# Kernel tuning notes

Measured on AMD Instinct MI355X. Metric: run time of the kernel, lower is better.

The kernel has to match this reference:

```python
import jax, jax.numpy as jnp
import numpy as np

B, L, V, E, RV, RD, H, C = 128, 256, 6000, 128, 300, 100, 256, 33
PAD, START, END = 0, 31, 32
DIN = E + 3 * RD  # 428, LSTM input size


def setup_inputs() -> dict:
    key = jax.random.key(0)
    ks = jax.random.split(key, 16)
    def n(k, shape, scale=0.05):
        return jax.random.normal(k, shape, jnp.float32) * scale
    batch_data = jax.random.randint(ks[0], (B, L), 0, V)
    batch_onerad = jax.random.randint(ks[1], (3, B, L), 0, RV)
    lengths = jax.random.randint(ks[2], (B,), L // 2, L + 1)
    tags = jax.random.randint(ks[3], (B, L), 1, C - 2)  # real tags, exclude PAD/START/END
    batch_tag = jnp.where(jnp.arange(L)[None, :] < lengths[:, None], tags, PAD)
    return dict(
        batch_data=batch_data, batch_onerad=batch_onerad, batch_tag=batch_tag,
        embed=n(ks[4], (V, E), 1.0), rad_embed=n(ks[5], (RV, RD), 1.0),
        Wih_f=n(ks[6], (4 * H, DIN)), Whh_f=n(ks[7], (4 * H, H)),
        bih_f=n(ks[8], (4 * H,)), bhh_f=n(ks[9], (4 * H,)),
        Wih_b=n(ks[10], (4 * H, DIN)), Whh_b=n(ks[11], (4 * H, H)),
        bih_b=n(ks[12], (4 * H,)), bhh_b=n(ks[13], (4 * H,)),
        Wcls=n(ks[14], (C, 2 * H)), bcls=n(ks[15], (C,)),
        transition=jnp.full((C, C), 1.0 / C, jnp.float32),
    )


def _lstm_dir(x, Wih, Whh, bih, bhh, reverse):
    # x: [B,L,D] -> h: [B,L,H]; PyTorch gate order i,f,g,o
    xg = jnp.einsum('bld,gd->blg', x, Wih) + bih + bhh  # [B,L,4H]
    xg = jnp.swapaxes(xg, 0, 1)  # [L,B,4H]
    h0 = jnp.zeros((x.shape[0], Whh.shape[1]), x.dtype)
    def step(carry, g):
        h, c = carry
        g = g + h @ Whh.T
        i, f, gg, o = jnp.split(g, 4, axis=-1)
        c = jax.nn.sigmoid(f) * c + jax.nn.sigmoid(i) * jnp.tanh(gg)
        h = jax.nn.sigmoid(o) * jnp.tanh(c)
        return (h, c), h
    _, hs = jax.lax.scan(step, (h0, h0), xg, reverse=reverse)
    return jnp.swapaxes(hs, 0, 1)


def _forward_loss(batch_data, batch_onerad, batch_tag, embed, rad_embed,
                  Wih_f, Whh_f, bih_f, bhh_f, Wih_b, Whh_b, bih_b, bhh_b,
                  Wcls, bcls, transition):
    emb = jnp.concatenate([embed[batch_data], rad_embed[batch_onerad[0]],
                           rad_embed[batch_onerad[1]], rad_embed[batch_onerad[2]]], axis=-1)
    hf = _lstm_dir(emb, Wih_f, Whh_f, bih_f, bhh_f, False)
    hb = _lstm_dir(emb, Wih_b, Whh_b, bih_b, bhh_b, True)
    out = jnp.concatenate([hf, hb], axis=-1)  # [B,L,2H]
    emission = out @ Wcls.T + bcls  # [B,L,C]
    crf_scores = emission[:, :, None, :] + transition  # [B,L,C_prev,C_cur]
    mask = batch_tag != PAD  # [B,L], padding only at the tail
    lengths = mask.sum(axis=1)  # [B]
    # golden path score: index prev*C + cur in flattened [C*C] per step
    prev = jnp.concatenate([jnp.full((B, 1), START, batch_tag.dtype), batch_tag[:, :-1]], axis=1)
    idx = prev * C + batch_tag  # [B,L]
    flat = crf_scores.reshape(B, L, C * C)
    golden = jnp.sum(jnp.take_along_axis(flat, idx[:, :, None], axis=2)[:, :, 0] * mask)
    # CRF forward algorithm (logsumexp scan over time)
    scores0 = jnp.where((lengths > 0)[:, None], crf_scores[:, 0, START, :], 0.0)  # [B,C]
    cs = jnp.swapaxes(crf_scores, 0, 1)[1:]  # [L-1,B,C,C]
    active = jnp.arange(1, L)[:, None] < lengths[None, :]  # [L-1,B]
    def fstep(scores, xs):
        cs_t, act = xs
        new = jax.nn.logsumexp(cs_t + scores[:, :, None], axis=1)  # reduce over prev tag
        return jnp.where(act[:, None], new, scores), None
    scores, _ = jax.lax.scan(fstep, scores0, (cs, active))
    all_path = scores[:, END].sum()
    return (all_path - golden) / B


def reference(batch_data, batch_onerad, batch_tag, embed, rad_embed,
              Wih_f, Whh_f, bih_f, bhh_f, Wih_b, Whh_b, bih_b, bhh_b,
              Wcls, bcls, transition):
    return _forward_loss(batch_data, batch_onerad, batch_tag, embed, rad_embed,
                         Wih_f, Whh_f, bih_f, bhh_f, Wih_b, Whh_b, bih_b, bhh_b,
                         Wcls, bcls, transition)
```

## Files before the change

### kernel.cpp

```cpp
#include <hip/hip_runtime.h>
#include <hip/hip_bf16.h>
#include <stdint.h>


typedef unsigned short u16;
typedef __attribute__((ext_vector_type(8))) __bf16 bf16x8;
typedef __attribute__((ext_vector_type(4))) float f32x4;
typedef __attribute__((ext_vector_type(8))) int i32x8;
typedef __attribute__((ext_vector_type(4))) int i32x4;

struct __align__(8) u16x4 { u16 x, y, z, w; };

typedef const void __attribute__((address_space(1))) gas_t;
typedef void __attribute__((address_space(3))) las_t;

static __device__ __forceinline__ void gload16(const void* g, void* l) {
  __builtin_amdgcn_global_load_lds((gas_t*)g, (las_t*)l, 16, 0, 0);
}

static __device__ __forceinline__ u16 f2b(float x) {
  uint32_t u = __builtin_bit_cast(uint32_t, x);
  uint32_t r = u + 0x7fffu + ((u >> 16) & 1u);
  return (u16)(r >> 16);
}
static __device__ __forceinline__ float b2lo(uint32_t u) {
  return __builtin_bit_cast(float, u << 16);
}
static __device__ __forceinline__ float b2hi(uint32_t u) {
  return __builtin_bit_cast(float, u & 0xffff0000u);
}
static __device__ __forceinline__ uint32_t pkbf16(float lo, float hi) {
  uint32_t w;
  asm("v_cvt_pk_bf16_f32 %0, %1, %2" : "=v"(w) : "v"(lo), "v"(hi));
  return w;
}
static __device__ __forceinline__ uint32_t pkf8x4(float x, float y, float z, float w) {
  unsigned int r01 = __builtin_amdgcn_cvt_pk_fp8_f32(x, y, 0u, false) & 0xffffu;
  unsigned int r23 = __builtin_amdgcn_cvt_pk_fp8_f32(z, w, 0u, false) & 0xffffu;
  return r01 | (r23 << 16);
}
static __device__ __forceinline__ float sigf(float x) {
  return __builtin_amdgcn_rcpf(1.f + __expf(-x));
}
static __device__ __forceinline__ float tanh_(float x) {
  return 1.f - 2.f * __builtin_amdgcn_rcpf(1.f + __expf(2.f * x));
}
static __device__ __forceinline__ f32x4 MFMA(bf16x8 a, bf16x8 b, f32x4 c) {
  return __builtin_amdgcn_mfma_f32_16x16x32_bf16(a, b, c, 0, 0, 0);
}

__global__ __launch_bounds__(256) void pack_all(
    const float* __restrict__ Wih_f, const float* __restrict__ Wih_b,
    const float* __restrict__ Whh_f, const float* __restrict__ Whh_b,
    const float* __restrict__ bih_f, const float* __restrict__ bhh_f,
    const float* __restrict__ bih_b, const float* __restrict__ bhh_b,
    const float* __restrict__ Wcls,
    const int* __restrict__ data, const int* __restrict__ onerad,
    const float* __restrict__ embed, const float* __restrict__ rad,
    unsigned char* __restrict__ W8, unsigned int* __restrict__ WhhF8,
    float* __restrict__ biasP, u16* __restrict__ WclsP,
    unsigned char* __restrict__ A8) {
  if (blockIdx.x < 1640) {
    int idx = blockIdx.x * 256 + threadIdx.x;
    if (idx < 262144) {
      int r = idx >> 7, c7 = idx & 127, k0 = c7 * 4;
      int d = r >> 10, rr = r & 1023;
      const float* W = d ? Wih_b : Wih_f;
      float4 f;
      if (k0 < 428) f = *(const float4*)(W + (size_t)rr * 428 + k0);
      else          f = make_float4(0.f, 0.f, 0.f, 0.f);
      *(unsigned int*)(W8 + (size_t)r * 512 + (k0 ^ ((r & 7) << 4))) =
          pkf8x4(f.x, f.y, f.z, f.w);
    } else if (idx < 264192) {
      int j = idx - 262144;
      int r = j & 1023;
      biasP[j] = (j >> 10) ? (bih_b[r] + bhh_b[r]) : (bih_f[r] + bhh_f[r]);
    } else if (idx < 288768) {
      int j = idx - 264192;
      int r = j >> 9, k = j & 511;
      WclsP[j] = (r < 33) ? f2b(Wcls[r * 512 + k]) : (u16)0;
    } else if (idx < 419840) {
      int q = idx - 288768;
      int f = q >> 9;
      int kt = f & 1, u = (f >> 1) & 7, v = (f >> 4) & 7, dd = f >> 7;
      int w9 = q & 511;
      int lane = w9 >> 3;
      int eb = (w9 & 7) * 4;
      int gate = u >> 1, jf = u & 1;
      int gcol = gate * 256 + v * 32 + jf * 16 + (lane & 15);
      int k = kt * 128 + (lane >> 4) * 32 + eb;
      const float* W = dd ? Whh_b : Whh_f;
      float4 fv4 = *(const float4*)(W + (size_t)gcol * 256 + k);
      WhhF8[q] = pkf8x4(fv4.x, fv4.y, fv4.z, fv4.w);
    }
  } else {
    int idx = (blockIdx.x - 1640) * 256 + threadIdx.x;
    int m = idx >> 7, c = idx & 127, k0 = c * 4;
    float4 vv;
    if (k0 < 128)      vv = *(const float4*)(embed + (size_t)data[m] * 128 + k0);
    else if (k0 < 228) vv = *(const float4*)(rad + (size_t)onerad[m] * 100 + (k0 - 128));
    else if (k0 < 328) vv = *(const float4*)(rad + (size_t)onerad[32768 + m] * 100 + (k0 - 228));
    else if (k0 < 428) vv = *(const float4*)(rad + (size_t)onerad[65536 + m] * 100 + (k0 - 328));
    else               vv = make_float4(0.f, 0.f, 0.f, 0.f);
    *(unsigned int*)(A8 + (size_t)m * 512 + (k0 ^ ((m & 7) << 4))) =
        pkf8x4(vv.x, vv.y, vv.z, vv.w);
  }
}

#define GXM(i, j) \
  acc[i][j] = __builtin_amdgcn_mfma_scale_f32_16x16x128_f8f6f4( \
      af[i], bfj, acc[i][j], 0, 0, 0, 0x7F7F7F7Fu, 0, 0x7F7F7F7Fu);
__global__ __launch_bounds__(256, 2) void gemm_xg(const unsigned char* __restrict__ A8,
    const unsigned char* __restrict__ W8, const float* __restrict__ bias,
    u16* __restrict__ X2) {
  __shared__ unsigned char As[16384];
  __shared__ unsigned char Bs[16384];
  int bid = blockIdx.x;
  int mt = bid >> 4, nt = bid & 15;
  int m0 = mt * 128, n0 = nt * 128;
  int tid = threadIdx.x;
  int w = tid >> 6, lane = tid & 63, l16 = lane & 15;
  int wr = w >> 1, wc = w & 1;
  int kc0 = (lane >> 4) * 32;
  f32x4 zero4 = {0.f, 0.f, 0.f, 0.f};
  f32x4 acc[4][4];
#pragma unroll
  for (int i = 0; i < 4; ++i)
#pragma unroll
    for (int j = 0; j < 4; ++j) acc[i][j] = zero4;
  for (int kk = 0; kk < 4; ++kk) {
    int kb = kk * 128;
#pragma unroll
    for (int ps = 0; ps < 4; ++ps) {
      int o = ps * 4096 + tid * 16;
      int rs = o >> 7, cb = o & 127;
      gload16(A8 + (size_t)(m0 + rs) * 512 + kb + cb, (char*)As + o);
      gload16(W8 + (size_t)(n0 + rs) * 512 + kb + cb, (char*)Bs + o);
    }
    __syncthreads();
    i32x8 af[4];
#pragma unroll
    for (int i = 0; i < 4; ++i) {
      int arow = wr * 64 + i * 16 + l16;
      int sw = (arow & 7) << 4;
      const unsigned char* ab = As + arow * 128;
      i32x4 x0 = *(const i32x4*)(ab + (kc0 ^ sw));
      i32x4 x1 = *(const i32x4*)(ab + ((kc0 + 16) ^ sw));
      af[i] = (i32x8){x0[0], x0[1], x0[2], x0[3], x1[0], x1[1], x1[2], x1[3]};
    }
#pragma unroll
    for (int j = 0; j < 4; ++j) {
      int brow = wc * 64 + j * 16 + l16;
      int sw = (brow & 7) << 4;
      const unsigned char* bb = Bs + brow * 128;
      i32x4 y0 = *(const i32x4*)(bb + (kc0 ^ sw));
      i32x4 y1 = *(const i32x4*)(bb + ((kc0 + 16) ^ sw));
      i32x8 bfj = (i32x8){y0[0], y0[1], y0[2], y0[3], y1[0], y1[1], y1[2], y1[3]};
      GXM(0, j) GXM(1, j) GXM(2, j) GXM(3, j)
    }
    __syncthreads();
  }
  float bv[4];
#pragma unroll
  for (int j = 0; j < 4; ++j) bv[j] = bias[n0 + wc * 64 + j * 16 + l16];
  int dd = n0 >> 10;
  int g = lane >> 4;
#pragma unroll
  for (int i = 0; i < 4; ++i)
#pragma unroll
    for (int jp = 0; jp < 2; ++jp) {
      int j0 = jp * 2;
      int c = (n0 + wc * 64 + j0 * 16 + l16) & 1023;
      int gate = c >> 8, vv = (c >> 5) & 7, lc = c & 15;
      size_t base = (size_t)dd * 33554432 + (size_t)gate * 256 + vv * 32 + lc * 2;
#pragma unroll
      for (int r = 0; r < 4; ++r) {
        int row = m0 + wr * 64 + i * 16 + g * 4 + r;
        *(unsigned int*)(X2 + base + (size_t)row * 1024) =
            pkbf16(acc[i][j0][r] + bv[j0], acc[i][j0 + 1][r] + bv[j0 + 1]);
      }
    }
}

#define MXM(u, Af, Bf) \
  acc[u] = __builtin_amdgcn_mfma_scale_f32_16x16x128_f8f6f4( \
      Af, Bf, acc[u], 0, 0, 0, 0x7F7F7F7Fu, 0, 0x7F7F7F7Fu);
#define GVAL(gate, dst) { \
  float a00 = __shfl(acc[(gate) * 2][0],     srcl); \
  float a01 = __shfl(acc[(gate) * 2][1],     srcl); \
  float a10 = __shfl(acc[(gate) * 2 + 1][0], srcl); \
  float a11 = __shfl(acc[(gate) * 2 + 1][1], srcl); \
  float s0 = hirow ? a01 : a00; \
  float s1 = hirow ? a11 : a10; \
  float xv = hijf ? b2hi(pxA[gate]) : b2lo(pxA[gate]); \
  dst = (hijf ? s1 : s0) + xv; }
#define FENCE { __builtin_amdgcn_sched_barrier(0); \
  asm volatile("s_waitcnt lgkmcnt(0)"); \
  __builtin_amdgcn_s_barrier(); \
  __builtin_amdgcn_sched_barrier(0); }

__global__ __launch_bounds__(512, 1) void lstm_recur(const u16* __restrict__ xg,
    const unsigned char* __restrict__ WhhF8, u16* __restrict__ outh) {
  __shared__ unsigned char hfA[2][4096];
  int blk = blockIdx.x;
  int d = blk >> 6, ch = blk & 63;
  int rowA0 = ch * 2;
  int tid = threadIdx.x;
  int v = tid >> 6, lane = tid & 63, l16 = lane & 15;
  int row = lane >> 5;
  int jf = (lane >> 4) & 1;
  bool hirow = (row == 1), hijf = (jf == 1);
  int srcl = l16;
  int col = v * 32 + jf * 16 + l16;

  const char* wb = (const char*)WhhF8 + (size_t)(d * 8 + v) * 32768 + (size_t)lane * 32;
  i32x8 bf0  = *(const i32x8*)(wb);
  i32x8 bf1  = *(const i32x8*)(wb + 2048);
  i32x8 bf2  = *(const i32x8*)(wb + 4096);
  i32x8 bf3  = *(const i32x8*)(wb + 6144);
  i32x8 bf4  = *(const i32x8*)(wb + 8192);
  i32x8 bf5  = *(const i32x8*)(wb + 10240);
  i32x8 bf6  = *(const i32x8*)(wb + 12288);
  i32x8 bf7  = *(const i32x8*)(wb + 14336);
  i32x8 bf8  = *(const i32x8*)(wb + 16384);
  i32x8 bf9  = *(const i32x8*)(wb + 18432);
  i32x8 bf10 = *(const i32x8*)(wb + 20480);
  i32x8 bf11 = *(const i32x8*)(wb + 22528);
  i32x8 bf12 = *(const i32x8*)(wb + 24576);
  i32x8 bf13 = *(const i32x8*)(wb + 26624);
  i32x8 bf14 = *(const i32x8*)(wb + 28672);
  i32x8 bf15 = *(const i32x8*)(wb + 30720);
  asm volatile("" :: "v"(bf0), "v"(bf1), "v"(bf2), "v"(bf3), "v"(bf4),
               "v"(bf5), "v"(bf6), "v"(bf7), "v"(bf8), "v"(bf9), "v"(bf10),
               "v"(bf11), "v"(bf12), "v"(bf13), "v"(bf14), "v"(bf15));

  for (int i = tid; i < 2048; i += 512) ((int*)hfA)[i] = 0;

  int arow = lane & 15;
  int sw = (arow & 7) << 4;
  int kb = (lane >> 4) * 32;
  int o0 = arow * 256 + ((kb) ^ sw);
  int o1 = arow * 256 + ((kb + 16) ^ sw);
  int o2 = arow * 256 + ((kb + 128) ^ sw);
  int o3 = arow * 256 + ((kb + 144) ^ sw);

  int t0 = d ? 255 : 0;
  int tpx = d ? -2048 : 2048;
  int tob = d ? -1024 : 1024;

  const char* pb = (const char*)xg + (size_t)d * 67108864
      + ((size_t)(rowA0 + row) * 256 + t0) * 2048 + v * 64 + l16 * 4;
  char* sb = (char*)outh
      + (((size_t)(rowA0 + row) * 256 + t0) * 512 + d * 256 + col) * 2;
  int fwoff = row * 256 + (col ^ (row << 4));

  unsigned int pxA[4];
  pxA[0] = *(const unsigned int*)(pb);
  pxA[1] = *(const unsigned int*)(pb + 512);
  pxA[2] = *(const unsigned int*)(pb + 1024);
  pxA[3] = *(const unsigned int*)(pb + 1536);

  asm volatile("s_waitcnt vmcnt(0)" ::: "memory");
  __builtin_amdgcn_sched_barrier(0);

  f32x4 zero4 = {0.f, 0.f, 0.f, 0.f};
  float cst = 0.f;
  f32x4 acc[8];
  __syncthreads();

#pragma unroll 1
  for (int tt = 0; tt < 256; ++tt) {
    int p = tt & 1;
    {
      const unsigned char* hb = &hfA[p][0];
      i32x4 a0 = *(const i32x4*)(hb + o0);
      i32x4 a1 = *(const i32x4*)(hb + o1);
      i32x4 a2 = *(const i32x4*)(hb + o2);
      i32x4 a3 = *(const i32x4*)(hb + o3);
      asm volatile("s_waitcnt lgkmcnt(0)");
      __builtin_amdgcn_sched_barrier(0);
      i32x8 A0 = {a0[0], a0[1], a0[2], a0[3], a1[0], a1[1], a1[2], a1[3]};
      i32x8 A1 = {a2[0], a2[1], a2[2], a2[3], a3[0], a3[1], a3[2], a3[3]};
      acc[0] = zero4; acc[1] = zero4; acc[2] = zero4; acc[3] = zero4;
      acc[4] = zero4; acc[5] = zero4; acc[6] = zero4; acc[7] = zero4;
      MXM(0, A0, bf0)  MXM(1, A0, bf2)  MXM(2, A0, bf4)  MXM(3, A0, bf6)
      MXM(4, A0, bf8)  MXM(5, A0, bf10) MXM(6, A0, bf12) MXM(7, A0, bf14)
      MXM(0, A1, bf1)  MXM(1, A1, bf3)  MXM(2, A1, bf5)  MXM(3, A1, bf7)
      MXM(4, A1, bf9)  MXM(5, A1, bf11) MXM(6, A1, bf13) MXM(7, A1, bf15)
    }
    {
      float iv, fv, gv, ov;
      GVAL(0, iv) GVAL(1, fv) GVAL(2, gv) GVAL(3, ov)
      float cn = sigf(fv) * cst + sigf(iv) * tanh_(gv);
      cst = cn;
      float hv = sigf(ov) * tanh_(cn);
      hfA[p ^ 1][fwoff] =
          (unsigned char)__builtin_amdgcn_cvt_pk_fp8_f32(hv, hv, 0u, false);
      *(u16*)sb = f2b(hv);
    }
    sb += tob; pb += tpx;
    pxA[0] = *(const unsigned int*)(pb);
    pxA[1] = *(const unsigned int*)(pb + 512);
    pxA[2] = *(const unsigned int*)(pb + 1024);
    pxA[3] = *(const unsigned int*)(pb + 1536);
    FENCE;
  }
}

__global__ __launch_bounds__(256) void emis_k(const u16* __restrict__ outh,
    const u16* __restrict__ WclsP, const float* __restrict__ bcls,
    float* __restrict__ emiB) {
  int tid = threadIdx.x;
  int w = tid >> 6, lane = tid & 63, l16 = lane & 15, g = lane >> 4;
  int mrow = blockIdx.x * 64 + w * 16;
  f32x4 zero4 = {0.f, 0.f, 0.f, 0.f};
  f32x4 acc[3] = {zero4, zero4, zero4};
#pragma unroll
  for (int kf = 0; kf < 16; ++kf) {
    bf16x8 a = *(const bf16x8*)(outh + (size_t)(mrow + l16) * 512 + kf * 32 + g * 8);
#pragma unroll
    for (int nf = 0; nf < 3; ++nf) {
      bf16x8 bb = *(const bf16x8*)(WclsP + (size_t)(nf * 16 + l16) * 512 + kf * 32 + g * 8);
      acc[nf] = MFMA(a, bb, acc[nf]);
    }
  }
#pragma unroll
  for (int nf = 0; nf < 3; ++nf) {
    int c = nf * 16 + l16;
    if (c < 33) {
      float bc = bcls[c];
#pragma unroll
      for (int r = 0; r < 4; ++r)
        emiB[(size_t)(mrow + g * 4 + r) * 33 + c] = acc[nf][r] + bc;
    }
  }
}

__global__ __launch_bounds__(64) void crf2_k(const int* __restrict__ tag,
    const float* __restrict__ emiB, const float* __restrict__ T,
    float* __restrict__ part) {
  int b = blockIdx.x;
  int lane = threadIdx.x;
  __shared__ float Ts[1089];
  __shared__ float E[8448];
  __shared__ float sc[33];
  for (int i = lane; i < 1089; i += 64) Ts[i] = T[i];
  {
    const float* eb = emiB + (size_t)b * 8448;
    for (int i = lane; i < 8448; i += 64) E[i] = eb[i];
  }
  int cnt = 0;
  for (int i = lane; i < 256; i += 64) cnt += (tag[b * 256 + i] != 0) ? 1 : 0;
#pragma unroll
  for (int o = 1; o < 64; o <<= 1) cnt += __shfl_xor(cnt, o);
  int len = cnt;
  __syncthreads();
  float gval = 0.f;
  for (int l = lane; l < 256; l += 64) {
    int tg = tag[b * 256 + l];
    if (tg != 0) {
      int prev = (l == 0) ? 31 : tag[b * 256 + l - 1];
      gval += E[l * 33 + tg] + Ts[prev * 33 + tg];
    }
  }
#pragma unroll
  for (int o = 32; o > 0; o >>= 1) gval += __shfl_down(gval, o);
  int c = lane;
  float tcol[33];
  if (c < 33) {
#pragma unroll
    for (int p = 0; p < 33; ++p) tcol[p] = Ts[p * 33 + c];
    sc[c] = E[c] + tcol[31];
  }
  __syncthreads();
#pragma unroll 1
  for (int t = 1; t < len; ++t) {
    float nv = 0.f;
    if (c < 33) {
      float ec = E[t * 33 + c];
      float vb[33];
      float m0 = -3.0e38f, m1 = -3.0e38f, m2 = -3.0e38f, m3 = -3.0e38f;
#pragma unroll
      for (int p = 0; p < 32; p += 4) {
        vb[p]     = sc[p]     + tcol[p];     m0 = fmaxf(m0, vb[p]);
        vb[p + 1] = sc[p + 1] + tcol[p + 1]; m1 = fmaxf(m1, vb[p + 1]);
        vb[p + 2] = sc[p + 2] + tcol[p + 2]; m2 = fmaxf(m2, vb[p + 2]);
        vb[p + 3] = sc[p + 3] + tcol[p + 3]; m3 = fmaxf(m3, vb[p + 3]);
      }
      vb[32] = sc[32] + tcol[32];
      float mx = fmaxf(fmaxf(fmaxf(m0, m1), fmaxf(m2, m3)), vb[32]);
      float s0 = 0.f, s1 = 0.f, s2 = 0.f, s3 = 0.f;
#pragma unroll
      for (int p = 0; p < 32; p += 4) {
        s0 += __expf(vb[p] - mx);     s1 += __expf(vb[p + 1] - mx);
        s2 += __expf(vb[p + 2] - mx); s3 += __expf(vb[p + 3] - mx);
      }
      s0 += __expf(vb[32] - mx);
      nv = ec + mx + __logf((s0 + s1) + (s2 + s3));
    }
    __syncthreads();
    if (c < 33) sc[c] = nv;
    __syncthreads();
  }
  if (lane == 0) part[b] = sc[32] - gval;
}

__global__ __launch_bounds__(64) void fin_k(const float* __restrict__ part,
    float* __restrict__ out) {
  int l = threadIdx.x;
  float v = part[l] + part[l + 64];
#pragma unroll
  for (int o = 32; o > 0; o >>= 1) v += __shfl_down(v, o);
  if (l == 0) out[0] = v / 128.f;
}

extern "C" void kernel_launch(void* const* d_in, const int* in_sizes, int n_in,
                              void* d_out, int out_size, void* d_ws, size_t ws_size,
                              hipStream_t stream) {
  const int*   batch_data   = (const int*)d_in[0];
  const int*   batch_onerad = (const int*)d_in[1];
  const int*   batch_tag    = (const int*)d_in[2];
  const float* embed        = (const float*)d_in[3];
  const float* rad_embed    = (const float*)d_in[4];
  const float* Wih_f = (const float*)d_in[5];
  const float* Whh_f = (const float*)d_in[6];
  const float* bih_f = (const float*)d_in[7];
  const float* bhh_f = (const float*)d_in[8];
  const float* Wih_b = (const float*)d_in[9];
  const float* Whh_b = (const float*)d_in[10];
  const float* bih_b = (const float*)d_in[11];
  const float* bhh_b = (const float*)d_in[12];
  const float* Wcls  = (const float*)d_in[13];
  const float* bcls  = (const float*)d_in[14];
  const float* trans = (const float*)d_in[15];

  char* ws = (char*)d_ws;
  unsigned char* A8 = (unsigned char*)(ws + 0);
  u16*   X2    = (u16*)  (ws + 29360128);
  unsigned char* W8 = (unsigned char*)(ws + 163577856);
  unsigned int* WhhF8 = (unsigned int*)(ws + 165412864);
  float* biasP = (float*)(ws + 165937152);
  u16*   WclsP = (u16*)  (ws + 165945344);
  u16*   outh  = (u16*)  (ws + 165994496);
  float* emiB  = (float*)(ws + 199548928);
  float* part  = (float*)(ws + 203874304);

  pack_all<<<18024, 256, 0, stream>>>(Wih_f, Wih_b, Whh_f, Whh_b, bih_f, bhh_f,
                                      bih_b, bhh_b, Wcls, batch_data, batch_onerad,
                                      embed, rad_embed, W8, WhhF8, biasP, WclsP, A8);
  gemm_xg<<<4096, 256, 0, stream>>>(A8, W8, biasP, X2);
  lstm_recur<<<128, 512, 0, stream>>>(X2, (const unsigned char*)WhhF8, outh);
  emis_k<<<512, 256, 0, stream>>>(outh, WclsP, bcls, emiB);
  crf2_k<<<128, 64, 0, stream>>>(batch_tag, emiB, trans, part);
  fin_k<<<1, 64, 0, stream>>>(part, (float*)d_out);
}
```

Baseline: 457.3 us.

## Fuse emission GEMM into CRF kernel and raise MFMA priority in LSTM

```diff
diff --git a/kernel.cpp b/kernel.cpp
--- a/kernel.cpp
+++ b/kernel.cpp
@@ -283,10 +283,12 @@
       i32x8 A1 = {a2[0], a2[1], a2[2], a2[3], a3[0], a3[1], a3[2], a3[3]};
       acc[0] = zero4; acc[1] = zero4; acc[2] = zero4; acc[3] = zero4;
       acc[4] = zero4; acc[5] = zero4; acc[6] = zero4; acc[7] = zero4;
+      __builtin_amdgcn_s_setprio(1);
       MXM(0, A0, bf0)  MXM(1, A0, bf2)  MXM(2, A0, bf4)  MXM(3, A0, bf6)
       MXM(4, A0, bf8)  MXM(5, A0, bf10) MXM(6, A0, bf12) MXM(7, A0, bf14)
       MXM(0, A1, bf1)  MXM(1, A1, bf3)  MXM(2, A1, bf5)  MXM(3, A1, bf7)
       MXM(4, A1, bf9)  MXM(5, A1, bf11) MXM(6, A1, bf13) MXM(7, A1, bf15)
+      __builtin_amdgcn_s_setprio(0);
     }
     {
       float iv, fv, gv, ov;
@@ -307,65 +309,76 @@
   }
 }
 
-__global__ __launch_bounds__(256) void emis_k(const u16* __restrict__ outh,
-    const u16* __restrict__ WclsP, const float* __restrict__ bcls,
-    float* __restrict__ emiB) {
-  int tid = threadIdx.x;
-  int w = tid >> 6, lane = tid & 63, l16 = lane & 15, g = lane >> 4;
-  int mrow = blockIdx.x * 64 + w * 16;
-  f32x4 zero4 = {0.f, 0.f, 0.f, 0.f};
-  f32x4 acc[3] = {zero4, zero4, zero4};
-#pragma unroll
-  for (int kf = 0; kf < 16; ++kf) {
-    bf16x8 a = *(const bf16x8*)(outh + (size_t)(mrow + l16) * 512 + kf * 32 + g * 8);
-#pragma unroll
-    for (int nf = 0; nf < 3; ++nf) {
-      bf16x8 bb = *(const bf16x8*)(WclsP + (size_t)(nf * 16 + l16) * 512 + kf * 32 + g * 8);
-      acc[nf] = MFMA(a, bb, acc[nf]);
-    }
-  }
-#pragma unroll
-  for (int nf = 0; nf < 3; ++nf) {
-    int c = nf * 16 + l16;
-    if (c < 33) {
-      float bc = bcls[c];
-#pragma unroll
-      for (int r = 0; r < 4; ++r)
-        emiB[(size_t)(mrow + g * 4 + r) * 33 + c] = acc[nf][r] + bc;
-    }
-  }
-}
-
-__global__ __launch_bounds__(64) void crf2_k(const int* __restrict__ tag,
-    const float* __restrict__ emiB, const float* __restrict__ T,
+__global__ __launch_bounds__(256) void crf3_k(const int* __restrict__ tag,
+    const u16* __restrict__ outh, const u16* __restrict__ WclsP,
+    const float* __restrict__ bcls, const float* __restrict__ T,
     float* __restrict__ part) {
-  int b = blockIdx.x;
-  int lane = threadIdx.x;
   __shared__ float Ts[1089];
   __shared__ float E[8448];
   __shared__ float sc[33];
-  for (int i = lane; i < 1089; i += 64) Ts[i] = T[i];
+  __shared__ int   lenS;
+  __shared__ float gS;
+  int b = blockIdx.x;
+  int tid = threadIdx.x;
+  int w = tid >> 6, lane = tid & 63, l16 = lane & 15, g = lane >> 4;
+  for (int i = tid; i < 1089; i += 256) Ts[i] = T[i];
   {
-    const float* eb = emiB + (size_t)b * 8448;
-    for (int i = lane; i < 8448; i += 64) E[i] = eb[i];
-  }
-  int cnt = 0;
-  for (int i = lane; i < 256; i += 64) cnt += (tag[b * 256 + i] != 0) ? 1 : 0;
-#pragma unroll
-  for (int o = 1; o < 64; o <<= 1) cnt += __shfl_xor(cnt, o);
-  int len = cnt;
+    f32x4 zero4 = {0.f, 0.f, 0.f, 0.f};
+    f32x4 acc[4][3];
+#pragma unroll
+    for (int mf = 0; mf < 4; ++mf)
+#pragma unroll
+      for (int nf = 0; nf < 3; ++nf) acc[mf][nf] = zero4;
+    int mbase = b * 256 + w * 64;
+#pragma unroll 1
+    for (int kf = 0; kf < 16; ++kf) {
+      bf16x8 bb[3];
+#pragma unroll
+      for (int nf = 0; nf < 3; ++nf)
+        bb[nf] = *(const bf16x8*)(WclsP + (size_t)(nf * 16 + l16) * 512 + kf * 32 + g * 8);
+#pragma unroll
+      for (int mf = 0; mf < 4; ++mf) {
+        bf16x8 a = *(const bf16x8*)(outh
+            + (size_t)(mbase + mf * 16 + l16) * 512 + kf * 32 + g * 8);
+#pragma unroll
+        for (int nf = 0; nf < 3; ++nf) acc[mf][nf] = MFMA(a, bb[nf], acc[mf][nf]);
+      }
+    }
+#pragma unroll
+    for (int nf = 0; nf < 3; ++nf) {
+      int c = nf * 16 + l16;
+      if (c < 33) {
+        float bc = bcls[c];
+#pragma unroll
+        for (int mf = 0; mf < 4; ++mf)
+#pragma unroll
+          for (int r = 0; r < 4; ++r)
+            E[(w * 64 + mf * 16 + g * 4 + r) * 33 + c] = acc[mf][nf][r] + bc;
+      }
+    }
+  }
+  if (w == 0) {
+    int cnt = 0;
+    for (int i = lane; i < 256; i += 64) cnt += (tag[b * 256 + i] != 0) ? 1 : 0;
+#pragma unroll
+    for (int o = 1; o < 64; o <<= 1) cnt += __shfl_xor(cnt, o);
+    if (lane == 0) lenS = cnt;
+  }
   __syncthreads();
-  float gval = 0.f;
-  for (int l = lane; l < 256; l += 64) {
-    int tg = tag[b * 256 + l];
-    if (tg != 0) {
-      int prev = (l == 0) ? 31 : tag[b * 256 + l - 1];
-      gval += E[l * 33 + tg] + Ts[prev * 33 + tg];
-    }
-  }
-#pragma unroll
-  for (int o = 32; o > 0; o >>= 1) gval += __shfl_down(gval, o);
-  int c = lane;
+  if (w == 0) {
+    float gval = 0.f;
+    for (int l = lane; l < 256; l += 64) {
+      int tg = tag[b * 256 + l];
+      if (tg != 0) {
+        int prev = (l == 0) ? 31 : tag[b * 256 + l - 1];
+        gval += E[l * 33 + tg] + Ts[prev * 33 + tg];
+      }
+    }
+#pragma unroll
+    for (int o = 32; o > 0; o >>= 1) gval += __shfl_down(gval, o);
+    if (lane == 0) gS = gval;
+  }
+  int c = tid;
   float tcol[33];
   if (c < 33) {
 #pragma unroll
@@ -373,6 +386,7 @@
     sc[c] = E[c] + tcol[31];
   }
   __syncthreads();
+  int len = lenS;
 #pragma unroll 1
   for (int t = 1; t < len; ++t) {
     float nv = 0.f;
@@ -402,7 +416,7 @@
     if (c < 33) sc[c] = nv;
     __syncthreads();
   }
-  if (lane == 0) part[b] = sc[32] - gval;
+  if (tid == 0) part[b] = sc[32] - gS;
 }
 
 __global__ __launch_bounds__(64) void fin_k(const float* __restrict__ part,
@@ -442,7 +456,6 @@
   float* biasP = (float*)(ws + 165937152);
   u16*   WclsP = (u16*)  (ws + 165945344);
   u16*   outh  = (u16*)  (ws + 165994496);
-  float* emiB  = (float*)(ws + 199548928);
   float* part  = (float*)(ws + 203874304);
 
   pack_all<<<18024, 256, 0, stream>>>(Wih_f, Wih_b, Whh_f, Whh_b, bih_f, bhh_f,
@@ -450,7 +463,6 @@
                                       embed, rad_embed, W8, WhhF8, biasP, WclsP, A8);
   gemm_xg<<<4096, 256, 0, stream>>>(A8, W8, biasP, X2);
   lstm_recur<<<128, 512, 0, stream>>>(X2, (const unsigned char*)WhhF8, outh);
-  emis_k<<<512, 256, 0, stream>>>(outh, WclsP, bcls, emiB);
-  crf2_k<<<128, 64, 0, stream>>>(batch_tag, emiB, trans, part);
+  crf3_k<<<128, 256, 0, stream>>>(batch_tag, outh, WclsP, bcls, trans, part);
   fin_k<<<1, 64, 0, stream>>>(part, (float*)d_out);
 }
```

Measured after the change: 461.6 us. No clear change (+0.9%).
